# Performance work log

Measured on AMD Instinct MI355X. Metric: run time of the kernel, lower is better.

## Reference

```python
import jax, jax.numpy as jnp
import numpy as np

DIM = 1024
N_STATE = 64
T, B = 512, 32


def _xavier(key, shape):
    fan_out, fan_in = shape
    limit = np.sqrt(6.0 / (fan_in + fan_out)).astype(np.float32)
    return jax.random.uniform(key, shape, jnp.float32, -limit, limit)


def setup_inputs() -> dict:
    key = jax.random.key(0)
    ks = jax.random.split(key, 5)
    return {
        "x": jax.random.normal(ks[0], (T, B, DIM), jnp.float32),
        "S": jnp.zeros((B, N_STATE, N_STATE), jnp.float32),
        "W_k": _xavier(ks[1], (N_STATE, DIM)),
        "W_v": _xavier(ks[2], (N_STATE, DIM)),
        "W_q": _xavier(ks[3], (N_STATE, DIM)),
        "W_alpha": _xavier(ks[4], (N_STATE, DIM)),
        "d_alpha": jnp.full((N_STATE,), 0.1, jnp.float32),
        "b_alpha": jnp.full((N_STATE,), 2.0, jnp.float32),
    }


def reference(x, S, W_k, W_v, W_q, W_alpha, d_alpha, b_alpha):
    # Precompute all projections as batched GEMMs: [T,B,n_state]
    k = jnp.einsum("tbd,nd->tbn", x, W_k)
    v = jnp.einsum("tbd,nd->tbn", x, W_v)
    q = jnp.einsum("tbd,nd->tbn", x, W_q)
    ax = jnp.einsum("tbd,nd->tbn", x, W_alpha)

    def step(S, inp):
        k_t, v_t, q_t, ax_t = inp  # each [B, n_state]
        retrieved = jnp.einsum("bij,bj->bi", S, k_t)          # S @ k
        alpha = jax.nn.sigmoid(ax_t + d_alpha * retrieved + b_alpha)
        # S = alpha * S + (1 - alpha) * outer(v, k); alpha gates rows
        S_new = alpha[:, :, None] * S + (1.0 - alpha)[:, :, None] * (
            v_t[:, :, None] * k_t[:, None, :]
        )
        h = jnp.einsum("bij,bj->bi", S_new, q_t)              # S @ q
        out_t = h * jax.nn.silu(h)                             # self-gated output
        return S_new, out_t

    S_final, output = jax.lax.scan(step, S, (k, v, q, ax))
    return output, S_final
```

## Files before the change

### kernel.cpp

```cpp
#include <hip/hip_runtime.h>
#include <hip/hip_bf16.h>

#define T_STEPS 512
#define BATCH 32
#define NST 64
#define DIM 1024

typedef _Float16 f16x8 __attribute__((ext_vector_type(8)));
typedef _Float16 f16x4 __attribute__((ext_vector_type(4)));
typedef float f32x4 __attribute__((ext_vector_type(4)));
typedef float f32x2 __attribute__((ext_vector_type(2)));

__device__ __forceinline__ void gl_lds16(const void* g, void* l) {
  __builtin_amdgcn_global_load_lds(
      (const __attribute__((address_space(1))) void*)g,
      (__attribute__((address_space(3))) void*)l, 16, 0, 0);
}

__global__ __launch_bounds__(256) void wconv(
    const float* __restrict__ Wk, const float* __restrict__ Wv,
    const float* __restrict__ Wq, const float* __restrict__ Wa,
    _Float16* __restrict__ Wc) {
  const int n = blockIdx.x;
  const int g = n >> 6, r = n & 63;
  const float* W = (g == 0) ? Wk : (g == 1) ? Wq : (g == 2) ? Wv : Wa;
  const float sc = (g == 3) ? -1.44269504088896340736f : 1.0f;
  float4 v = *(const float4*)(W + (size_t)r * DIM + threadIdx.x * 4);
  f16x4 h = {(_Float16)(v.x * sc), (_Float16)(v.y * sc), (_Float16)(v.z * sc),
             (_Float16)(v.w * sc)};
  *(f16x4*)(Wc + (size_t)n * DIM + threadIdx.x * 4) = h;
}

__global__ __launch_bounds__(512) void proj_gemm(
    const float* __restrict__ x, const _Float16* __restrict__ Wc,
    float* __restrict__ projf) {
  const int m0 = blockIdx.x * 64;
  const int tid = threadIdx.x;
  const int lane = tid & 63, wv = tid >> 6;
  const int wm = wv >> 2, wn = wv & 3;
  const int fm = lane & 15, fq = lane >> 4;

  __shared__ __align__(16) _Float16 Bl[2][256 * 32];
  __shared__ __align__(16) _Float16 Al[2][64 * 32];

  const int brow = tid >> 2;
  const int bcg = (tid & 3) ^ ((tid >> 3) & 3);
  const _Float16* gB = Wc + (size_t)brow * DIM + bcg * 8;
  const int bdst = tid * 8;

#define STAGE_B(buf, k0)                                          \
  {                                                               \
    _Pragma("unroll") for (int i = 0; i < 2; ++i)                 \
        gl_lds16(gB + (size_t)i * 128 * DIM + (k0),               \
                 &Bl[buf][i * 4096 + bdst]);                      \
  }

  const int arow = tid >> 3;
  const int afc = (tid & 7) * 4;
  const float* gA = x + (size_t)(m0 + arow) * DIM + afc;
  const int awp = arow * 32 + ((((tid >> 1) & 3) ^ ((arow >> 1) & 3)) * 8) +
                  (tid & 1) * 4;

#define LOADX(rr, k0)                          \
  {                                            \
    rr = *(const float4*)(gA + (k0));          \
  }
#define CVT_WRITE_A(buf, rr)                                        \
  {                                                                 \
    f16x4 h = {(_Float16)rr.x, (_Float16)rr.y, (_Float16)rr.z,      \
               (_Float16)rr.w};                                     \
    *(f16x4*)&Al[buf][awp] = h;                                     \
  }

  f32x4 acc[2][4];
#pragma unroll
  for (int mi = 0; mi < 2; ++mi)
#pragma unroll
    for (int ni = 0; ni < 4; ++ni) acc[mi][ni] = (f32x4){0.f, 0.f, 0.f, 0.f};

  const int aswz = (fq ^ ((fm >> 1) & 3)) * 8;
  const int abase = (wm * 32 + fm) * 32 + aswz;
  const int bbase = (wn * 64 + fm) * 32 + aswz;

#define COMPUTE(cb)                                                     \
  {                                                                     \
    f16x8 afr[2], bfr[4];                                               \
    _Pragma("unroll") for (int mi = 0; mi < 2; ++mi)                    \
        afr[mi] = *(const f16x8*)&Al[cb][abase + mi * 16 * 32];         \
    _Pragma("unroll") for (int ni = 0; ni < 4; ++ni)                    \
        bfr[ni] = *(const f16x8*)&Bl[cb][bbase + ni * 16 * 32];         \
    _Pragma("unroll") for (int mi = 0; mi < 2; ++mi)                    \
        _Pragma("unroll") for (int ni = 0; ni < 4; ++ni)                \
            acc[mi][ni] = __builtin_amdgcn_mfma_f32_16x16x32_f16(       \
                afr[mi], bfr[ni], acc[mi][ni], 0, 0, 0);                \
  }

  float4 rE, rO;
  LOADX(rE, 0);
  STAGE_B(0, 0);
  LOADX(rO, 32);
  CVT_WRITE_A(0, rE);
  __syncthreads();

  for (int k2 = 0; k2 < 16; ++k2) {
    STAGE_B(1, (2 * k2 + 1) * 32);
    if (k2 < 15) LOADX(rE, (2 * k2 + 2) * 32);
    CVT_WRITE_A(1, rO);
    COMPUTE(0);
    __syncthreads();
    if (k2 < 15) {
      STAGE_B(0, (2 * k2 + 2) * 32);
      LOADX(rO, (2 * k2 + 3) * 32);
      CVT_WRITE_A(0, rE);
    }
    COMPUTE(1);
    __syncthreads();
  }
#undef STAGE_B
#undef LOADX
#undef CVT_WRITE_A
#undef COMPUTE

#pragma unroll
  for (int mi = 0; mi < 2; ++mi)
#pragma unroll
    for (int ni = 0; ni < 4; ++ni) {
      const int gcol = wn * 64 + ni * 16 + fm;
      const int pcol = gcol < 128 ? gcol
                     : (gcol < 192 ? 128 + 2 * (gcol - 128) : 129 + 2 * (gcol - 192));
#pragma unroll
      for (int r = 0; r < 4; ++r) {
        const int grow = m0 + wm * 32 + mi * 16 + fq * 4 + r;
        projf[(size_t)grow * 256 + pcol] = acc[mi][ni][r];
      }
    }
}

__device__ __forceinline__ float red16(float x) {
  int v = __builtin_amdgcn_update_dpp(0, __float_as_int(x), 0xB1, 0xF, 0xF, true);
  x += __int_as_float(v);
  v = __builtin_amdgcn_update_dpp(0, __float_as_int(x), 0x4E, 0xF, 0xF, true);
  x += __int_as_float(v);
  v = __builtin_amdgcn_update_dpp(0, __float_as_int(x), 0x124, 0xF, 0xF, true);
  x += __int_as_float(v);
  v = __builtin_amdgcn_update_dpp(0, __float_as_int(x), 0x128, 0xF, 0xF, true);
  x += __int_as_float(v);
  return x;
}

__global__ __launch_bounds__(512, 1) void scan_kernel(
    const float* __restrict__ projf, const float* __restrict__ S0,
    const float* __restrict__ d_alpha, const float* __restrict__ b_alpha,
    float* __restrict__ out, float* __restrict__ Sout) {
  const int b = blockIdx.x >> 2;
  const int rg = blockIdx.x & 3;
  const int tid = threadIdx.x;
  const bool prod = tid < 256;
  const int ptid = tid & 255;
  const int c = ptid & 15;
  const int lr = ptid >> 4;
  const int r = rg * 16 + lr;
  const int j0 = c * 4;

  __shared__ __align__(16) float2 alcc[2][16][8];

  constexpr float NL2E = -1.44269504088896340736f;
  f32x2 s01, s23;
  {
    float4 v = *(const float4*)(S0 + ((size_t)b * NST + r) * NST + j0);
    s01 = (f32x2){v.x, v.y}; s23 = (f32x2){v.z, v.w};
  }
  const float da2 = d_alpha[r] * NL2E;
  const float ba2 = b_alpha[r] * NL2E;

  const float* gb = projf + (size_t)b * 256;

#define P_LOAD(karr, varr, chn)                                         \
  {                                                                     \
    const float* pb = gb + (size_t)(chn) * 65536;                       \
    _Pragma("unroll") for (int si = 0; si < 8; ++si) {                  \
      karr[si] = *(const float4*)(pb + si * 8192 + j0);                 \
      varr[si] = *(const float2*)(pb + si * 8192 + 128 + 2 * r);        \
    }                                                                   \
  }
#define C_LOAD(karr, qarr, chn)                                         \
  {                                                                     \
    const float* pb = gb + (size_t)(chn) * 65536;                       \
    _Pragma("unroll") for (int si = 0; si < 8; ++si) {                  \
      karr[si] = *(const float4*)(pb + si * 8192 + j0);                 \
      qarr[si] = *(const float4*)(pb + si * 8192 + 64 + j0);            \
    }                                                                   \
  }

#define P_COMP(karr, varr, abuf)                                        \
  {                                                                     \
    _Pragma("unroll") for (int si = 0; si < 8; ++si) {                  \
      const f32x2 k01 = {karr[si].x, karr[si].y};                       \
      const f32x2 k23 = {karr[si].z, karr[si].w};                       \
      f32x2 pa = s01 * k01 + s23 * k23;                                 \
      const float rr = red16(pa[0] + pa[1]);                            \
      float z2 = fmaf(da2, rr, varr[si].y + ba2);                       \
      z2 = __builtin_amdgcn_fmed3f(z2, -43.3f, 43.3f);                  \
      const float e = __builtin_amdgcn_exp2f(z2);                       \
      const float al = __builtin_amdgcn_rcpf(1.f + e);                  \
      const float ccv = (e * varr[si].x) * al;                          \
      const f32x2 al2 = {al, al}, cc2 = {ccv, ccv};                     \
      s01 = al2 * s01 + cc2 * k01;                                      \
      s23 = al2 * s23 + cc2 * k23;                                      \
      if (c == 0) alcc[abuf][lr][si] = make_float2(al, ccv);            \
    }                                                                   \
  }
#define C_COMP(karr, qarr, abuf, chn)                                   \
  {                                                                     \
    float2 acv[8];                                                      \
    _Pragma("unroll") for (int si = 0; si < 8; ++si)                    \
        acv[si] = alcc[abuf][lr][si];                                   \
    _Pragma("unroll") for (int si = 0; si < 8; ++si) {                  \
      const f32x2 k01 = {karr[si].x, karr[si].y};                       \
      const f32x2 k23 = {karr[si].z, karr[si].w};                       \
      const f32x2 al2 = {acv[si].x, acv[si].x};                         \
      const f32x2 cc2 = {acv[si].y, acv[si].y};                         \
      s01 = al2 * s01 + cc2 * k01;                                      \
      s23 = al2 * s23 + cc2 * k23;                                      \
      const f32x2 q01 = {qarr[si].x, qarr[si].y};                       \
      const f32x2 q23 = {qarr[si].z, qarr[si].w};                       \
      f32x2 hh = s01 * q01 + s23 * q23;                                 \
      const float h = red16(hh[0] + hh[1]);                             \
      if (c == 0) {                                                     \
        const float sg =                                                \
            __builtin_amdgcn_rcpf(1.f + __builtin_amdgcn_exp2f(h * NL2E)); \
        out[((size_t)((chn) * 8 + si) * BATCH + b) * NST + r] = (h * h) * sg; \
      }                                                                 \
    }                                                                   \
  }

  float4 kA[8], kB[8];
  float2 vA[8], vB[8];
  float4 qA[8], qB[8];

  if (prod) {
    P_LOAD(kA, vA, 0);
  }

  for (int c2 = 0; c2 < 32; ++c2) {
    if (prod) {
      P_LOAD(kB, vB, 2 * c2 + 1);
      P_COMP(kA, vA, 0);
    } else {
      C_LOAD(kA, qA, 2 * c2);
      if (c2 > 0) C_COMP(kB, qB, 1, 2 * c2 - 1);
    }
    __syncthreads();
    if (prod) {
      if (c2 < 31) P_LOAD(kA, vA, 2 * c2 + 2);
      P_COMP(kB, vB, 1);
    } else {
      C_LOAD(kB, qB, 2 * c2 + 1);
      C_COMP(kA, qA, 0, 2 * c2);
    }
    __syncthreads();
  }
  if (!prod) {
    C_COMP(kB, qB, 1, 63);
    float4 o = {s01[0], s01[1], s23[0], s23[1]};
    *(float4*)(Sout + ((size_t)b * NST + r) * NST + j0) = o;
  }
#undef P_LOAD
#undef C_LOAD
#undef P_COMP
#undef C_COMP
}

extern "C" void kernel_launch(void* const* d_in, const int* in_sizes, int n_in,
                              void* d_out, int out_size, void* d_ws, size_t ws_size,
                              hipStream_t stream) {
  const float* x  = (const float*)d_in[0];
  const float* S0 = (const float*)d_in[1];
  const float* Wk = (const float*)d_in[2];
  const float* Wv = (const float*)d_in[3];
  const float* Wq = (const float*)d_in[4];
  const float* Wa = (const float*)d_in[5];
  const float* da = (const float*)d_in[6];
  const float* ba = (const float*)d_in[7];

  float* out  = (float*)d_out;
  float* Sout = out + (size_t)T_STEPS * BATCH * NST;
  float* projf = (float*)d_ws;
  _Float16* Wc = (_Float16*)((char*)d_ws + (size_t)16384 * 256 * 4);

  wconv<<<256, 256, 0, stream>>>(Wk, Wv, Wq, Wa, Wc);
  proj_gemm<<<256, 512, 0, stream>>>(x, Wc, projf);
  scan_kernel<<<4 * BATCH, 512, 0, stream>>>(projf, S0, da, ba, out, Sout);
}
```

Measured before the change: 237.7 us.

## Stage projection chunks through LDS ring buffer with cooperative coalesced loads

Replaces per-thread strided global loads of k/v/q for each chunk with a cooperative, coalesced float4 staging of each 8-step chunk into a 4-slot LDS ring buffer loaded two chunks ahead. Producer and consumer threads then read their slices from LDS. It also reorders the alpha update algebra, batches alpha/cc writes into vector LDS stores, and defers output stores by one chunk. The aim is to cut global-load latency on the serial scan's critical path, at the cost of 32KB of LDS and extra LDS traffic.

```diff
diff --git a/kernel.cpp b/kernel.cpp
--- a/kernel.cpp
+++ b/kernel.cpp
@@ -162,6 +162,7 @@
   const int r = rg * 16 + lr;
   const int j0 = c * 4;
 
+  __shared__ __align__(16) float lbuf[4][2048];
   __shared__ __align__(16) float2 alcc[2][16][8];
 
   constexpr float NL2E = -1.44269504088896340736f;
@@ -173,102 +174,145 @@
   const float da2 = d_alpha[r] * NL2E;
   const float ba2 = b_alpha[r] * NL2E;
 
-  const float* gb = projf + (size_t)b * 256;
-
-#define P_LOAD(karr, varr, chn)                                         \
-  {                                                                     \
-    const float* pb = gb + (size_t)(chn) * 65536;                       \
+  const int sstep = tid >> 6;
+  const int soff = (tid & 63) * 4;
+  const int lidx = sstep * 256 + soff;
+  const float* gp = projf + (size_t)b * 256;
+#define GADDR(ch) (gp + (size_t)((ch) * 8 + sstep) * (BATCH * 256) + soff)
+
+  float4 kA[8], kB[8];
+  float2 vA[8], vB[8];
+  float4 qA[8], qB[8];
+  float ys[8];
+
+#define P_PREF(kX, vX, slot)                                            \
+  {                                                                     \
+    const float* Pn = &lbuf[slot][0];                                   \
     _Pragma("unroll") for (int si = 0; si < 8; ++si) {                  \
-      karr[si] = *(const float4*)(pb + si * 8192 + j0);                 \
-      varr[si] = *(const float2*)(pb + si * 8192 + 128 + 2 * r);        \
-    }                                                                   \
-  }
-#define C_LOAD(karr, qarr, chn)                                         \
-  {                                                                     \
-    const float* pb = gb + (size_t)(chn) * 65536;                       \
+      kX[si] = *(const float4*)(Pn + si * 256 + j0);                    \
+      vX[si] = *(const float2*)(Pn + si * 256 + 128 + 2 * r);           \
+    }                                                                   \
+  }
+#define C_PREF(kX, qX, slot)                                            \
+  {                                                                     \
+    const float* Pn = &lbuf[slot][0];                                   \
     _Pragma("unroll") for (int si = 0; si < 8; ++si) {                  \
-      karr[si] = *(const float4*)(pb + si * 8192 + j0);                 \
-      qarr[si] = *(const float4*)(pb + si * 8192 + 64 + j0);            \
-    }                                                                   \
-  }
-
-#define P_COMP(karr, varr, abuf)                                        \
-  {                                                                     \
+      kX[si] = *(const float4*)(Pn + si * 256 + j0);                    \
+      qX[si] = *(const float4*)(Pn + si * 256 + 64 + j0);               \
+    }                                                                   \
+  }
+#define P_COMP(kX, vX, abuf)                                            \
+  {                                                                     \
+    float alv[8], ccv[8];                                               \
     _Pragma("unroll") for (int si = 0; si < 8; ++si) {                  \
-      const f32x2 k01 = {karr[si].x, karr[si].y};                       \
-      const f32x2 k23 = {karr[si].z, karr[si].w};                       \
+      const f32x2 k01 = {kX[si].x, kX[si].y};                           \
+      const f32x2 k23 = {kX[si].z, kX[si].w};                           \
       f32x2 pa = s01 * k01 + s23 * k23;                                 \
       const float rr = red16(pa[0] + pa[1]);                            \
-      float z2 = fmaf(da2, rr, varr[si].y + ba2);                       \
+      float z2 = fmaf(da2, rr, vX[si].y + ba2);                         \
       z2 = __builtin_amdgcn_fmed3f(z2, -43.3f, 43.3f);                  \
-      const float e = __builtin_amdgcn_exp2f(z2);                       \
-      const float al = __builtin_amdgcn_rcpf(1.f + e);                  \
-      const float ccv = (e * varr[si].x) * al;                          \
-      const f32x2 al2 = {al, al}, cc2 = {ccv, ccv};                     \
-      s01 = al2 * s01 + cc2 * k01;                                      \
-      s23 = al2 * s23 + cc2 * k23;                                      \
-      if (c == 0) alcc[abuf][lr][si] = make_float2(al, ccv);            \
-    }                                                                   \
-  }
-#define C_COMP(karr, qarr, abuf, chn)                                   \
-  {                                                                     \
+      const float e = __builtin_amdgcn_exp2f(z2);          \
+      const float ev = e * vX[si].x;                                    \
+      const f32x2 ev2 = {ev, ev};                                       \
+      const f32x2 w01 = s01 + ev2 * k01;         \
+      const f32x2 w23 = s23 + ev2 * k23;                                \
+      const float al = __builtin_amdgcn_rcpf(1.f + e);     \
+      const f32x2 al2 = {al, al};                                       \
+      s01 = al2 * w01;                         \
+      s23 = al2 * w23;                                                  \
+      alv[si] = al; ccv[si] = al * ev;               \
+    }                                                                   \
+    if (c == 0) {                                                       \
+      float4 w0 = {alv[0], ccv[0], alv[1], ccv[1]};                     \
+      float4 w1 = {alv[2], ccv[2], alv[3], ccv[3]};                     \
+      float4 w2 = {alv[4], ccv[4], alv[5], ccv[5]};                     \
+      float4 w3 = {alv[6], ccv[6], alv[7], ccv[7]};                     \
+      float4* wp = (float4*)&alcc[abuf][lr][0];                         \
+      wp[0] = w0; wp[1] = w1; wp[2] = w2; wp[3] = w3;                   \
+    }                                                                   \
+  }
+#define C_COMP(kX, qX, abuf)                                            \
+  {                                                                     \
+    const float4* ap = (const float4*)&alcc[abuf][lr][0];               \
+    float4 a0 = ap[0], a1 = ap[1], a2 = ap[2], a3 = ap[3];              \
     float2 acv[8];                                                      \
-    _Pragma("unroll") for (int si = 0; si < 8; ++si)                    \
-        acv[si] = alcc[abuf][lr][si];                                   \
+    acv[0] = make_float2(a0.x, a0.y); acv[1] = make_float2(a0.z, a0.w); \
+    acv[2] = make_float2(a1.x, a1.y); acv[3] = make_float2(a1.z, a1.w); \
+    acv[4] = make_float2(a2.x, a2.y); acv[5] = make_float2(a2.z, a2.w); \
+    acv[6] = make_float2(a3.x, a3.y); acv[7] = make_float2(a3.z, a3.w); \
     _Pragma("unroll") for (int si = 0; si < 8; ++si) {                  \
-      const f32x2 k01 = {karr[si].x, karr[si].y};                       \
-      const f32x2 k23 = {karr[si].z, karr[si].w};                       \
+      const f32x2 k01 = {kX[si].x, kX[si].y};                           \
+      const f32x2 k23 = {kX[si].z, kX[si].w};                           \
       const f32x2 al2 = {acv[si].x, acv[si].x};                         \
       const f32x2 cc2 = {acv[si].y, acv[si].y};                         \
       s01 = al2 * s01 + cc2 * k01;                                      \
       s23 = al2 * s23 + cc2 * k23;                                      \
-      const f32x2 q01 = {qarr[si].x, qarr[si].y};                       \
-      const f32x2 q23 = {qarr[si].z, qarr[si].w};                       \
+      const f32x2 q01 = {qX[si].x, qX[si].y};                           \
+      const f32x2 q23 = {qX[si].z, qX[si].w};                           \
       f32x2 hh = s01 * q01 + s23 * q23;                                 \
       const float h = red16(hh[0] + hh[1]);                             \
-      if (c == 0) {                                                     \
-        const float sg =                                                \
-            __builtin_amdgcn_rcpf(1.f + __builtin_amdgcn_exp2f(h * NL2E)); \
-        out[((size_t)((chn) * 8 + si) * BATCH + b) * NST + r] = (h * h) * sg; \
-      }                                                                 \
-    }                                                                   \
-  }
-
-  float4 kA[8], kB[8];
-  float2 vA[8], vB[8];
-  float4 qA[8], qB[8];
-
-  if (prod) {
-    P_LOAD(kA, vA, 0);
-  }
+      const float sg =                                                  \
+          __builtin_amdgcn_rcpf(1.f + __builtin_amdgcn_exp2f(h * NL2E)); \
+      ys[si] = (h * h) * sg;                                            \
+    }                                                                   \
+  }
+#define C_STORE(pc)                                                     \
+  {                                                                     \
+    if (c == 0) {                                                       \
+      _Pragma("unroll") for (int si = 0; si < 8; ++si)                  \
+          out[((size_t)((pc) * 8 + si) * BATCH + b) * NST + r] = ys[si]; \
+    }                                                                   \
+  }
+
+  float4 rA;
+  rA = *(const float4*)GADDR(0); *(float4*)&lbuf[0][lidx] = rA;
+  rA = *(const float4*)GADDR(1); *(float4*)&lbuf[1][lidx] = rA;
+  __syncthreads();
+  if (prod) P_PREF(kA, vA, 0);
 
   for (int c2 = 0; c2 < 32; ++c2) {
-    if (prod) {
-      P_LOAD(kB, vB, 2 * c2 + 1);
-      P_COMP(kA, vA, 0);
-    } else {
-      C_LOAD(kA, qA, 2 * c2);
-      if (c2 > 0) C_COMP(kB, qB, 1, 2 * c2 - 1);
+    {
+      const int ch = 2 * c2;
+      if (ch + 2 < 64) rA = *(const float4*)GADDR(ch + 2);
+      if (prod) {
+        if (ch + 1 < 64) P_PREF(kB, vB, (ch + 1) & 3);
+        P_COMP(kA, vA, 0);
+      } else {
+        if (ch >= 2) C_STORE(ch - 2);
+        if (ch >= 1) C_COMP(kB, qB, 1);
+        C_PREF(kA, qA, ch & 3);
+      }
+      if (ch + 2 < 64) *(float4*)&lbuf[(ch + 2) & 3][lidx] = rA;
+      __syncthreads();
     }
-    __syncthreads();
-    if (prod) {
-      if (c2 < 31) P_LOAD(kA, vA, 2 * c2 + 2);
-      P_COMP(kB, vB, 1);
-    } else {
-      C_LOAD(kB, qB, 2 * c2 + 1);
-      C_COMP(kA, qA, 0, 2 * c2);
+    {
+      const int ch = 2 * c2 + 1;
+      if (ch + 2 < 64) rA = *(const float4*)GADDR(ch + 2);
+      if (prod) {
+        if (ch + 1 < 64) P_PREF(kA, vA, (ch + 1) & 3);
+        P_COMP(kB, vB, 1);
+      } else {
+        if (ch >= 2) C_STORE(ch - 2);
+        C_COMP(kA, qA, 0);
+        C_PREF(kB, qB, ch & 3);
+      }
+      if (ch + 2 < 64) *(float4*)&lbuf[(ch + 2) & 3][lidx] = rA;
+      __syncthreads();
     }
-    __syncthreads();
   }
   if (!prod) {
-    C_COMP(kB, qB, 1, 63);
+    C_STORE(62);
+    C_COMP(kB, qB, 1);
+    C_STORE(63);
     float4 o = {s01[0], s01[1], s23[0], s23[1]};
     *(float4*)(Sout + ((size_t)b * NST + r) * NST + j0) = o;
   }
-#undef P_LOAD
-#undef C_LOAD
+#undef GADDR
+#undef P_PREF
+#undef C_PREF
 #undef P_COMP
 #undef C_COMP
+#undef C_STORE
 }
 
 extern "C" void kernel_launch(void* const* d_in, const int* in_sizes, int n_in,
```

Result: faster. 204.8 us (-13.8%).
